# Kernel optimization log

Measured on AMD Instinct MI355X. Metric: run time of the kernel, lower is better.

The kernel has to match this reference:

```python
import jax, jax.numpy as jnp
import numpy as np

B, L, H, DK, DV, DM = 8, 1024, 8, 80, 80, 640
LN_EPS = 1e-5


def setup_inputs() -> dict:
    key = jax.random.key(0)
    ks = jax.random.split(key, 5)
    q = jax.random.normal(ks[0], (B, L, DM), dtype=jnp.float32)
    k = jax.random.normal(ks[1], (B, L, DM), dtype=jnp.float32)
    v = jax.random.normal(ks[2], (B, L, DM), dtype=jnp.float32)
    # fc: nn.Linear(n_head*d_v, d_model), xavier-normal init
    fc_std = float(np.sqrt(2.0 / (H * DV + DM)))
    fc_w = jax.random.normal(ks[3], (DM, H * DV), dtype=jnp.float32) * fc_std
    fc_b = jnp.zeros((DM,), dtype=jnp.float32)
    gamma_1 = jnp.full((DM,), 1e-4, dtype=jnp.float32)  # init_values * ones(640)
    ln_w = jnp.ones((DM,), dtype=jnp.float32)
    ln_b = jnp.zeros((DM,), dtype=jnp.float32)
    return {"q": q, "k": k, "v": v, "fc_w": fc_w, "fc_b": fc_b,
            "gamma_1": gamma_1, "ln_w": ln_w, "ln_b": ln_b}


def reference(q, k, v, fc_w, fc_b, gamma_1, ln_w, ln_b):
    # Inputs are viewed directly into heads (projections are commented out in source).
    residual = q
    qh = q.reshape(B, L, H, DK)  # [b, q, h, d]
    kh = k.reshape(B, L, H, DK)  # [b, k, h, d]
    vh = v.reshape(B, L, H, DV)  # [b, k, h, d]

    # L2-distance attention scores: -sum((q-k)^2) = -(||q||^2 - 2 q.k + ||k||^2)
    sq = jnp.sum(qh * qh, axis=-1)                       # [b, q, h]
    sk = jnp.sum(kh * kh, axis=-1)                       # [b, k, h]
    cross = jnp.einsum('bqhd,bkhd->bhqk', qh, kh)        # [b, h, q, k]
    scores = -(sq.transpose(0, 2, 1)[:, :, :, None]
               - 2.0 * cross
               + sk.transpose(0, 2, 1)[:, :, None, :]) / 13.0

    attn = jax.nn.softmax(scores, axis=-1)               # softmax over keys (dim=2 in 3D view)
    # dropout(p=0.8) treated as identity (eval mode)

    out = jnp.einsum('bhqk,bkhd->bqhd', attn, vh)        # [b, q, h, dv]
    out = out.reshape(B, L, H * DV)
    out = out @ fc_w.T + fc_b                            # fc projection
    # dropout treated as identity (eval mode)

    x = out * gamma_1 + residual
    mu = jnp.mean(x, axis=-1, keepdims=True)
    var = jnp.mean((x - mu) ** 2, axis=-1, keepdims=True)
    y = (x - mu) * jax.lax.rsqrt(var + LN_EPS) * ln_w + ln_b
    return y
```

## Files before the change

kernel.cpp:

```cpp
#include <hip/hip_runtime.h>

#define B_ 8
#define L_ 1024
#define H_ 8
#define DM_ 640

typedef __attribute__((ext_vector_type(8))) short bf16x8;
typedef __attribute__((ext_vector_type(4))) short bf16x4;
typedef __attribute__((ext_vector_type(4))) float f32x4;
typedef __attribute__((ext_vector_type(2))) float f32x2;
typedef __attribute__((ext_vector_type(4))) int i32x4;
typedef __attribute__((ext_vector_type(2))) int i32x2;
typedef __attribute__((ext_vector_type(4))) unsigned short us4;
typedef __attribute__((ext_vector_type(8))) unsigned short us8;

#if __has_builtin(__builtin_amdgcn_exp2f)
#define EXP2F __builtin_amdgcn_exp2f
#else
#define EXP2F exp2f
#endif

#define C1F 0.22195308f
#define C2F 0.11097654f

#define VTP_TILE_SHORTS 5184
#define ATTN8_OFF 10616832

__device__ __forceinline__ unsigned short f2bf(float f) {
  unsigned int u = __builtin_bit_cast(unsigned int, f);
  u += 0x7fffu + ((u >> 16) & 1u);
  return (unsigned short)(u >> 16);
}
__device__ __forceinline__ float bf2f(unsigned short h) {
  unsigned int u = ((unsigned int)h) << 16;
  return __builtin_bit_cast(float, u);
}
__device__ __forceinline__ float sane(float x, float lim) {
  return fminf(fmaxf(x, -lim), lim);
}

__global__ __launch_bounds__(256) void prep_kernel(
    const float* __restrict__ kg, const float* __restrict__ vg,
    unsigned short* __restrict__ Kp, unsigned short* __restrict__ Vtp) {
  __shared__ float V_lds[64 * 81];
  __shared__ float w_lds[64];
  const int tid = threadIdx.x;
  const int bh = blockIdx.x >> 4, kt = blockIdx.x & 15;
  const int b = bh >> 3, h = bh & 7;
  const int key = tid >> 2, part = tid & 3;
  const int keyg = kt * 64 + key;

  const float* krow = kg + (size_t)(b * L_ + keyg) * DM_ + h * 80 + part * 20;
  const float* vrow = vg + (size_t)(b * L_ + keyg) * DM_ + h * 80 + part * 20;
  unsigned short* kpr = Kp + ((size_t)bh * L_ + keyg) * 80 + part * 20;

  float ssq = 0.f;
#pragma unroll
  for (int i = 0; i < 5; ++i) {
    float4 f = *(const float4*)(krow + 4 * i);
    ssq += f.x * f.x + f.y * f.y + f.z * f.z + f.w * f.w;
    us4 h4 = {f2bf(f.x * C1F), f2bf(f.y * C1F), f2bf(f.z * C1F), f2bf(f.w * C1F)};
    *(us4*)(kpr + 4 * i) = h4;
    float4 g4 = *(const float4*)(vrow + 4 * i);
    int d0 = part * 20 + 4 * i;
    V_lds[key * 81 + d0 + 0] = g4.x;
    V_lds[key * 81 + d0 + 1] = g4.y;
    V_lds[key * 81 + d0 + 2] = g4.z;
    V_lds[key * 81 + d0 + 3] = g4.w;
  }
  ssq += __shfl_xor(ssq, 1);
  ssq += __shfl_xor(ssq, 2);
  if (part == 0) w_lds[key] = EXP2F((80.f - ssq) * C2F);
  __syncthreads();

  unsigned short* vt = Vtp + (size_t)(bh * 16 + kt) * VTP_TILE_SHORTS;
#pragma unroll
  for (int r = 0; r < 11; ++r) {
    int p = r * 256 + tid;
    if (p < 81 * 32) {
      int dv = p >> 5, kp = (p & 31) * 2;
      float wa = w_lds[kp], wb = w_lds[kp + 1];
      float va = (dv < 80) ? V_lds[kp * 81 + dv] * wa : wa;
      float vb = (dv < 80) ? V_lds[(kp + 1) * 81 + dv] * wb : wb;
      *(unsigned*)(vt + dv * 64 + kp) =
          (unsigned)f2bf(va) | ((unsigned)f2bf(vb) << 16);
    }
  }
}

#define KSTR 104
#define VSTR 72

__global__ __launch_bounds__(512) void attn_kernel(
    const float* __restrict__ qg, const unsigned short* __restrict__ Kp,
    const unsigned short* __restrict__ Vtp, unsigned char* __restrict__ attn8) {
  __shared__ __align__(16) unsigned short K_lds[2][64 * KSTR];
  __shared__ __align__(16) unsigned short Vt_lds[2][96 * VSTR];

  const int tid = threadIdx.x;
  const int wid = tid >> 6, lane = tid & 63;
  const int col = lane & 15, g = lane >> 4;
  const int g1 = g & 1, g2 = g >> 1;
  const int bx = blockIdx.x;
  const int bh = bx & 63, qt = bx >> 6;
  const int b = bh >> 3, h = bh & 7;

  {
    us8 z = {0, 0, 0, 0, 0, 0, 0, 0};
    if (tid < 128) {
      int bufz = tid >> 6, r = tid & 63;
      *(us8*)&K_lds[bufz][r * KSTR + 80] = z;
      *(us8*)&K_lds[bufz][r * KSTR + 88] = z;
    }
    if (tid < 240) {
      int bufz = tid / 120, t2 = tid % 120;
      int vr = 81 + (t2 >> 3), hc = t2 & 7;
      *(us8*)&Vt_lds[bufz][vr * VSTR + hc * 8] = z;
    }
  }

  const int kr0 = tid / 10, kc0 = tid - kr0 * 10;
  const int idx1 = tid + 512;
  const int kr1 = idx1 / 10, kc1 = idx1 - kr1 * 10;
  const int vr0 = tid >> 3, vc0 = tid & 7;
  const int vr1 = idx1 >> 3, vc1 = idx1 & 7;

  const unsigned short* kslice = Kp + (size_t)bh * L_ * 80;
  const unsigned short* vslice = Vtp + (size_t)(bh * 16) * VTP_TILE_SHORTS;

  us8 sk0, sk1, sv0, sv1;
  auto load_tile = [&](int kt) {
    const unsigned short* kb = kslice + (size_t)kt * 5120;
    const unsigned short* vb = vslice + (size_t)kt * VTP_TILE_SHORTS;
    sk0 = *(const us8*)(kb + kr0 * 80 + kc0 * 8);
    if (tid < 128) sk1 = *(const us8*)(kb + kr1 * 80 + kc1 * 8);
    sv0 = *(const us8*)(vb + vr0 * 64 + vc0 * 8);
    if (tid < 136) sv1 = *(const us8*)(vb + vr1 * 64 + vc1 * 8);
  };
  auto write_tile = [&](int bf) {
    *(us8*)&K_lds[bf][kr0 * KSTR + kc0 * 8] = sk0;
    if (tid < 128) *(us8*)&K_lds[bf][kr1 * KSTR + kc1 * 8] = sk1;
    *(us8*)&Vt_lds[bf][vr0 * VSTR + vc0 * 8] = sv0;
    if (tid < 136) *(us8*)&Vt_lds[bf][vr1 * VSTR + vc1 * 8] = sv1;
  };

  bf16x8 qa[3];
  {
    const int qrow = qt * 128 + wid * 16 + col;
    const float* qr = qg + (size_t)(b * L_ + qrow) * DM_ + h * 80;
#pragma unroll
    for (int c = 0; c < 3; ++c) {
      int d0 = c * 32 + g * 8;
      if (d0 < 80) {
        float4 f0 = *(const float4*)(qr + d0);
        float4 f1 = *(const float4*)(qr + d0 + 4);
        qa[c][0] = (short)f2bf(f0.x); qa[c][1] = (short)f2bf(f0.y);
        qa[c][2] = (short)f2bf(f0.z); qa[c][3] = (short)f2bf(f0.w);
        qa[c][4] = (short)f2bf(f1.x); qa[c][5] = (short)f2bf(f1.y);
        qa[c][6] = (short)f2bf(f1.z); qa[c][7] = (short)f2bf(f1.w);
      } else {
#pragma unroll
        for (int e = 0; e < 8; ++e) qa[c][e] = 0;
      }
    }
  }

  f32x4 acc_o[6];
#pragma unroll
  for (int u = 0; u < 6; ++u) {
    f32x4 z = {0.f, 0.f, 0.f, 0.f};
    acc_o[u] = z;
  }

  load_tile(0);
  write_tile(0);
  __syncthreads();

  for (int kt = 0; kt < 16; ++kt) {
    const int cur = kt & 1;
    if (kt < 15) load_tile(kt + 1);

    f32x4 accS[4];
#pragma unroll
    for (int t = 0; t < 4; ++t) {
      f32x4 z = {0.f, 0.f, 0.f, 0.f};
      accS[t] = z;
    }
#pragma unroll
    for (int t = 0; t < 4; ++t)
#pragma unroll
      for (int c = 0; c < 3; ++c) {
        bf16x8 kf =
            *(const bf16x8*)&K_lds[cur][(t * 16 + col) * KSTR + c * 32 + g * 8];
        accS[t] = __builtin_amdgcn_mfma_f32_16x16x32_bf16(kf, qa[c], accS[t], 0, 0, 0);
      }

    unsigned pkA[4], pkB[4];
#pragma unroll
    for (int t = 0; t < 4; ++t) {
      float p0 = EXP2F(accS[t][0]);
      float p1 = EXP2F(accS[t][1]);
      float p2 = EXP2F(accS[t][2]);
      float p3 = EXP2F(accS[t][3]);
      pkA[t] = (unsigned)f2bf(p0) | ((unsigned)f2bf(p1) << 16);
      pkB[t] = (unsigned)f2bf(p2) | ((unsigned)f2bf(p3) << 16);
    }

#if __has_builtin(__builtin_amdgcn_mfma_f32_16x16x16bf16_1k)
#pragma unroll
    for (int t = 0; t < 4; ++t) {
      i32x2 pw = {(int)pkA[t], (int)pkB[t]};
      bf16x4 pf = __builtin_bit_cast(bf16x4, pw);
#pragma unroll
      for (int u = 0; u < 6; ++u) {
        bf16x4 vf =
            *(const bf16x4*)&Vt_lds[cur][(u * 16 + col) * VSTR + t * 16 + g * 4];
        acc_o[u] =
            __builtin_amdgcn_mfma_f32_16x16x16bf16_1k(vf, pf, acc_o[u], 0, 0, 0);
      }
    }
#else
#pragma unroll
    for (int c = 0; c < 2; ++c) {
      int A0 = pkA[2 * c], A1 = pkA[2 * c + 1];
      int B0 = pkB[2 * c], B1 = pkB[2 * c + 1];
      int a16 = __shfl_xor(A0, 16), a32 = __shfl_xor(A0, 32), a48 = __shfl_xor(A0, 48);
      int c16 = __shfl_xor(A1, 16), c32 = __shfl_xor(A1, 32), c48 = __shfl_xor(A1, 48);
      int b16 = __shfl_xor(B0, 16), b32 = __shfl_xor(B0, 32), b48 = __shfl_xor(B0, 48);
      int d16 = __shfl_xor(B1, 16), d32 = __shfl_xor(B1, 32), d48 = __shfl_xor(B1, 48);
      int W0 = g2 ? (g1 ? c16 : c32) : (g1 ? a48 : A0);
      int W1 = g2 ? (g1 ? d16 : d32) : (g1 ? b48 : B0);
      int W2 = g2 ? (g1 ? A1 : c48) : (g1 ? a32 : a16);
      int W3 = g2 ? (g1 ? B1 : d48) : (g1 ? b32 : b16);
      i32x4 wv = {W0, W1, W2, W3};
      bf16x8 pf = __builtin_bit_cast(bf16x8, wv);
#pragma unroll
      for (int u = 0; u < 6; ++u) {
        bf16x8 vf =
            *(const bf16x8*)&Vt_lds[cur][(u * 16 + col) * VSTR + c * 32 + g * 8];
        acc_o[u] = __builtin_amdgcn_mfma_f32_16x16x32_bf16(vf, pf, acc_o[u], 0, 0, 0);
      }
    }
#endif

    if (kt < 15) {
      write_tile(cur ^ 1);
      __syncthreads();
    }
  }

  float l = __shfl(acc_o[5][0], col);
  float invl = 1.0f / fmaxf(l, 1e-30f);
  const int qrow = qt * 128 + wid * 16 + col;
  unsigned char* ob = attn8 + (size_t)(b * L_ + qrow) * DM_ + h * 80;
#pragma unroll
  for (int u = 0; u < 5; ++u) {
    float o0 = sane(acc_o[u][0] * invl, 240.f);
    float o1 = sane(acc_o[u][1] * invl, 240.f);
    float o2 = sane(acc_o[u][2] * invl, 240.f);
    float o3 = sane(acc_o[u][3] * invl, 240.f);
    int pk = __builtin_amdgcn_cvt_pk_fp8_f32(o0, o1, 0, false);
    pk = __builtin_amdgcn_cvt_pk_fp8_f32(o2, o3, pk, true);
    *(int*)(ob + u * 16 + g * 4) = pk;
  }
}

#define BSTR 40
__global__ __launch_bounds__(256) void fc_kernel(
    const unsigned char* __restrict__ attn8, const float* __restrict__ w,
    const float* __restrict__ fcb, const float* __restrict__ gamma,
    const float* __restrict__ qres, unsigned short* __restrict__ xout) {
  __shared__ __align__(16) unsigned short A_lds[128 * BSTR];
  __shared__ __align__(16) unsigned short B_lds[128 * BSTR];

  const int tid = threadIdx.x;
  const int wid = tid >> 6, lane = tid & 63;
  const int col = lane & 15, g = lane >> 4;
  const int rt = blockIdx.x / 5, ct = blockIdx.x % 5;
  const int wm = wid >> 1, wn = wid & 1;

  f32x4 acc[4][4];
#pragma unroll
  for (int m = 0; m < 4; ++m)
#pragma unroll
    for (int n = 0; n < 4; ++n) {
      f32x4 z = {0.f, 0.f, 0.f, 0.f};
      acc[m][n] = z;
    }

  for (int kc = 0; kc < 20; ++kc) {
    __syncthreads();
    {
      const int r = tid >> 1, seg = tid & 1;
      const unsigned char* as =
          attn8 + (size_t)(rt * 128 + r) * DM_ + kc * 32 + seg * 16;
      uint4 a4 = *(const uint4*)as;
      const unsigned* adw = (const unsigned*)&a4;
#pragma unroll
      for (int wde = 0; wde < 4; ++wde) {
        f32x2 lo = __builtin_amdgcn_cvt_pk_f32_fp8(adw[wde], false);
        f32x2 hi = __builtin_amdgcn_cvt_pk_f32_fp8(adw[wde], true);
        us4 h4 = {f2bf(lo[0]), f2bf(lo[1]), f2bf(hi[0]), f2bf(hi[1])};
        *(us4*)&A_lds[r * BSTR + seg * 16 + wde * 4] = h4;
      }
      const float* wsrc = w + (size_t)(ct * 128 + r) * DM_ + kc * 32 + seg * 16;
#pragma unroll
      for (int i = 0; i < 4; ++i) {
        float4 f = *(const float4*)(wsrc + 4 * i);
        us4 h4 = {f2bf(f.x), f2bf(f.y), f2bf(f.z), f2bf(f.w)};
        *(us4*)&B_lds[r * BSTR + seg * 16 + 4 * i] = h4;
      }
    }
    __syncthreads();

    bf16x8 af[4], bfr[4];
#pragma unroll
    for (int m = 0; m < 4; ++m)
      af[m] = *(const bf16x8*)&A_lds[(wm * 64 + m * 16 + col) * BSTR + g * 8];
#pragma unroll
    for (int n = 0; n < 4; ++n)
      bfr[n] = *(const bf16x8*)&B_lds[(wn * 64 + n * 16 + col) * BSTR + g * 8];
#pragma unroll
    for (int m = 0; m < 4; ++m)
#pragma unroll
      for (int n = 0; n < 4; ++n)
        acc[m][n] = __builtin_amdgcn_mfma_f32_16x16x32_bf16(af[m], bfr[n], acc[m][n], 0, 0, 0);
  }

  int jcol[4];
  float fb4[4], gm[4];
#pragma unroll
  for (int n = 0; n < 4; ++n) {
    jcol[n] = ct * 128 + wn * 64 + n * 16 + col;
    fb4[n] = fcb[jcol[n]];
    gm[n] = gamma[jcol[n]];
  }
#pragma unroll
  for (int m = 0; m < 4; ++m) {
    int rowg = rt * 128 + wm * 64 + m * 16 + g * 4;
#pragma unroll
    for (int j = 0; j < 4; ++j) {
      int row = rowg + j;
#pragma unroll
      for (int n = 0; n < 4; ++n) {
        float xv = (acc[m][n][j] + fb4[n]) * gm[n] + qres[(size_t)row * DM_ + jcol[n]];
        xout[(size_t)row * DM_ + jcol[n]] = f2bf(sane(xv, 1e5f));
      }
    }
  }
}

__global__ __launch_bounds__(256) void ln_kernel(
    const unsigned short* __restrict__ x, const float* __restrict__ lw,
    const float* __restrict__ lb, float* __restrict__ y) {
  const int wid = threadIdx.x >> 6, lane = threadIdx.x & 63;
  const int row = blockIdx.x * 4 + wid;
  const unsigned short* xr = x + (size_t)row * DM_;

  unsigned int u[5];
  float s = 0.f, ss = 0.f;
#pragma unroll
  for (int i = 0; i < 5; ++i) {
    u[i] = *(const unsigned int*)(xr + 2 * (lane + 64 * i));
    float a0 = bf2f((unsigned short)(u[i] & 0xffff));
    float a1 = bf2f((unsigned short)(u[i] >> 16));
    s += a0 + a1;
    ss += a0 * a0 + a1 * a1;
  }
#pragma unroll
  for (int d = 1; d < 64; d <<= 1) {
    s += __shfl_xor(s, d);
    ss += __shfl_xor(ss, d);
  }
  const float mu = s * (1.f / 640.f);
  const float var = ss * (1.f / 640.f) - mu * mu;
  const float rstd = rsqrtf(var + 1e-5f);

  float* yr = y + (size_t)row * DM_;
#pragma unroll
  for (int i = 0; i < 5; ++i) {
    int c0 = 2 * (lane + 64 * i);
    float a0 = bf2f((unsigned short)(u[i] & 0xffff));
    float a1 = bf2f((unsigned short)(u[i] >> 16));
    float2 wv = *(const float2*)(lw + c0);
    float2 bv = *(const float2*)(lb + c0);
    float2 out;
    out.x = (a0 - mu) * rstd * wv.x + bv.x;
    out.y = (a1 - mu) * rstd * wv.y + bv.y;
    *(float2*)(yr + c0) = out;
  }
}

extern "C" void kernel_launch(void* const* d_in, const int* in_sizes, int n_in,
                              void* d_out, int out_size, void* d_ws, size_t ws_size,
                              hipStream_t stream) {
  const float* q = (const float*)d_in[0];
  const float* k = (const float*)d_in[1];
  const float* v = (const float*)d_in[2];
  const float* fw = (const float*)d_in[3];
  const float* fb = (const float*)d_in[4];
  const float* g1 = (const float*)d_in[5];
  const float* lw = (const float*)d_in[6];
  const float* lb = (const float*)d_in[7];

  unsigned short* vtp = (unsigned short*)d_out;
  unsigned char* attn8 = (unsigned char*)d_out + ATTN8_OFF;
  unsigned short* kp = (unsigned short*)d_ws;
  unsigned short* xws = (unsigned short*)d_ws;
  float* y = (float*)d_out;

  prep_kernel<<<dim3(64 * 16), dim3(256), 0, stream>>>(k, v, kp, vtp);
  attn_kernel<<<dim3(64 * 8), dim3(512), 0, stream>>>(q, kp, vtp, attn8);
  fc_kernel<<<dim3((8192 / 128) * 5), dim3(256), 0, stream>>>(attn8, fw, fb, g1, q, xws);
  ln_kernel<<<dim3(8192 / 4), dim3(256), 0, stream>>>(xws, lw, lb, y);
}
```

Measured before the change: 100.9 us.

## Process two query tiles per attention block and double-buffer fc LDS tiles

The attention kernel now handles 256 query rows per block, two 128-row sets sharing each K/V tile loaded into LDS. This halves K/V global and LDS traffic per query, and the grid is halved to 256 blocks. The fc kernel gains double-buffered LDS with register prefetch of the next k-chunk, and the V LDS stride changes from 72 to 76 with a launch-bounds occupancy hint. The trade-off is more registers per thread and fewer blocks (256 on a many-CU GPU), which may underfill the device.

```diff
diff --git a/kernel.cpp b/kernel.cpp
--- a/kernel.cpp
+++ b/kernel.cpp
@@ -89,9 +89,9 @@
 }
 
 #define KSTR 104
-#define VSTR 72
-
-__global__ __launch_bounds__(512) void attn_kernel(
+#define VSTR 76
+
+__global__ __launch_bounds__(512, 2) void attn_kernel(
     const float* __restrict__ qg, const unsigned short* __restrict__ Kp,
     const unsigned short* __restrict__ Vtp, unsigned char* __restrict__ attn8) {
   __shared__ __align__(16) unsigned short K_lds[2][64 * KSTR];
@@ -100,7 +100,6 @@
   const int tid = threadIdx.x;
   const int wid = tid >> 6, lane = tid & 63;
   const int col = lane & 15, g = lane >> 4;
-  const int g1 = g & 1, g2 = g >> 1;
   const int bx = blockIdx.x;
   const int bh = bx & 63, qt = bx >> 6;
   const int b = bh >> 3, h = bh & 7;
@@ -144,32 +143,37 @@
     if (tid < 136) *(us8*)&Vt_lds[bf][vr1 * VSTR + vc1 * 8] = sv1;
   };
 
-  bf16x8 qa[3];
+  bf16x8 qa0[3], qa1[3];
   {
-    const int qrow = qt * 128 + wid * 16 + col;
-    const float* qr = qg + (size_t)(b * L_ + qrow) * DM_ + h * 80;
-#pragma unroll
-    for (int c = 0; c < 3; ++c) {
-      int d0 = c * 32 + g * 8;
-      if (d0 < 80) {
-        float4 f0 = *(const float4*)(qr + d0);
-        float4 f1 = *(const float4*)(qr + d0 + 4);
-        qa[c][0] = (short)f2bf(f0.x); qa[c][1] = (short)f2bf(f0.y);
-        qa[c][2] = (short)f2bf(f0.z); qa[c][3] = (short)f2bf(f0.w);
-        qa[c][4] = (short)f2bf(f1.x); qa[c][5] = (short)f2bf(f1.y);
-        qa[c][6] = (short)f2bf(f1.z); qa[c][7] = (short)f2bf(f1.w);
-      } else {
-#pragma unroll
-        for (int e = 0; e < 8; ++e) qa[c][e] = 0;
+    const int qr0 = qt * 256 + wid * 16 + col;
+#pragma unroll
+    for (int s = 0; s < 2; ++s) {
+      const float* qr = qg + (size_t)(b * L_ + qr0 + s * 128) * DM_ + h * 80;
+      bf16x8* qa = s ? qa1 : qa0;
+#pragma unroll
+      for (int c = 0; c < 3; ++c) {
+        int d0 = c * 32 + g * 8;
+        if (d0 < 80) {
+          float4 f0 = *(const float4*)(qr + d0);
+          float4 f1 = *(const float4*)(qr + d0 + 4);
+          qa[c][0] = (short)f2bf(f0.x); qa[c][1] = (short)f2bf(f0.y);
+          qa[c][2] = (short)f2bf(f0.z); qa[c][3] = (short)f2bf(f0.w);
+          qa[c][4] = (short)f2bf(f1.x); qa[c][5] = (short)f2bf(f1.y);
+          qa[c][6] = (short)f2bf(f1.z); qa[c][7] = (short)f2bf(f1.w);
+        } else {
+#pragma unroll
+          for (int e = 0; e < 8; ++e) qa[c][e] = 0;
+        }
       }
     }
   }
 
-  f32x4 acc_o[6];
+  f32x4 acc_o0[6], acc_o1[6];
 #pragma unroll
   for (int u = 0; u < 6; ++u) {
     f32x4 z = {0.f, 0.f, 0.f, 0.f};
-    acc_o[u] = z;
+    acc_o0[u] = z;
+    acc_o1[u] = z;
   }
 
   load_tile(0);
@@ -180,11 +184,12 @@
     const int cur = kt & 1;
     if (kt < 15) load_tile(kt + 1);
 
-    f32x4 accS[4];
+    f32x4 accS0[4], accS1[4];
 #pragma unroll
     for (int t = 0; t < 4; ++t) {
       f32x4 z = {0.f, 0.f, 0.f, 0.f};
-      accS[t] = z;
+      accS0[t] = z;
+      accS1[t] = z;
     }
 #pragma unroll
     for (int t = 0; t < 4; ++t)
@@ -192,53 +197,65 @@
       for (int c = 0; c < 3; ++c) {
         bf16x8 kf =
             *(const bf16x8*)&K_lds[cur][(t * 16 + col) * KSTR + c * 32 + g * 8];
-        accS[t] = __builtin_amdgcn_mfma_f32_16x16x32_bf16(kf, qa[c], accS[t], 0, 0, 0);
+        accS0[t] = __builtin_amdgcn_mfma_f32_16x16x32_bf16(kf, qa0[c], accS0[t], 0, 0, 0);
+        accS1[t] = __builtin_amdgcn_mfma_f32_16x16x32_bf16(kf, qa1[c], accS1[t], 0, 0, 0);
       }
 
-    unsigned pkA[4], pkB[4];
+    unsigned pkA0[4], pkB0[4], pkA1[4], pkB1[4];
 #pragma unroll
     for (int t = 0; t < 4; ++t) {
-      float p0 = EXP2F(accS[t][0]);
-      float p1 = EXP2F(accS[t][1]);
-      float p2 = EXP2F(accS[t][2]);
-      float p3 = EXP2F(accS[t][3]);
-      pkA[t] = (unsigned)f2bf(p0) | ((unsigned)f2bf(p1) << 16);
-      pkB[t] = (unsigned)f2bf(p2) | ((unsigned)f2bf(p3) << 16);
+      pkA0[t] = (unsigned)f2bf(EXP2F(accS0[t][0])) |
+                ((unsigned)f2bf(EXP2F(accS0[t][1])) << 16);
+      pkB0[t] = (unsigned)f2bf(EXP2F(accS0[t][2])) |
+                ((unsigned)f2bf(EXP2F(accS0[t][3])) << 16);
+      pkA1[t] = (unsigned)f2bf(EXP2F(accS1[t][0])) |
+                ((unsigned)f2bf(EXP2F(accS1[t][1])) << 16);
+      pkB1[t] = (unsigned)f2bf(EXP2F(accS1[t][2])) |
+                ((unsigned)f2bf(EXP2F(accS1[t][3])) << 16);
     }
 
 #if __has_builtin(__builtin_amdgcn_mfma_f32_16x16x16bf16_1k)
 #pragma unroll
     for (int t = 0; t < 4; ++t) {
-      i32x2 pw = {(int)pkA[t], (int)pkB[t]};
-      bf16x4 pf = __builtin_bit_cast(bf16x4, pw);
+      i32x2 pw0 = {(int)pkA0[t], (int)pkB0[t]};
+      i32x2 pw1 = {(int)pkA1[t], (int)pkB1[t]};
+      bf16x4 pf0 = __builtin_bit_cast(bf16x4, pw0);
+      bf16x4 pf1 = __builtin_bit_cast(bf16x4, pw1);
 #pragma unroll
       for (int u = 0; u < 6; ++u) {
         bf16x4 vf =
             *(const bf16x4*)&Vt_lds[cur][(u * 16 + col) * VSTR + t * 16 + g * 4];
-        acc_o[u] =
-            __builtin_amdgcn_mfma_f32_16x16x16bf16_1k(vf, pf, acc_o[u], 0, 0, 0);
+        acc_o0[u] = __builtin_amdgcn_mfma_f32_16x16x16bf16_1k(vf, pf0, acc_o0[u], 0, 0, 0);
+        acc_o1[u] = __builtin_amdgcn_mfma_f32_16x16x16bf16_1k(vf, pf1, acc_o1[u], 0, 0, 0);
       }
     }
 #else
-#pragma unroll
-    for (int c = 0; c < 2; ++c) {
-      int A0 = pkA[2 * c], A1 = pkA[2 * c + 1];
-      int B0 = pkB[2 * c], B1 = pkB[2 * c + 1];
-      int a16 = __shfl_xor(A0, 16), a32 = __shfl_xor(A0, 32), a48 = __shfl_xor(A0, 48);
-      int c16 = __shfl_xor(A1, 16), c32 = __shfl_xor(A1, 32), c48 = __shfl_xor(A1, 48);
-      int b16 = __shfl_xor(B0, 16), b32 = __shfl_xor(B0, 32), b48 = __shfl_xor(B0, 48);
-      int d16 = __shfl_xor(B1, 16), d32 = __shfl_xor(B1, 32), d48 = __shfl_xor(B1, 48);
-      int W0 = g2 ? (g1 ? c16 : c32) : (g1 ? a48 : A0);
-      int W1 = g2 ? (g1 ? d16 : d32) : (g1 ? b48 : B0);
-      int W2 = g2 ? (g1 ? A1 : c48) : (g1 ? a32 : a16);
-      int W3 = g2 ? (g1 ? B1 : d48) : (g1 ? b32 : b16);
-      i32x4 wv = {W0, W1, W2, W3};
-      bf16x8 pf = __builtin_bit_cast(bf16x8, wv);
-#pragma unroll
-      for (int u = 0; u < 6; ++u) {
-        bf16x8 vf =
-            *(const bf16x8*)&Vt_lds[cur][(u * 16 + col) * VSTR + c * 32 + g * 8];
-        acc_o[u] = __builtin_amdgcn_mfma_f32_16x16x32_bf16(vf, pf, acc_o[u], 0, 0, 0);
+    const int g1 = g & 1, g2 = g >> 1;
+#pragma unroll
+    for (int s = 0; s < 2; ++s) {
+      unsigned* pkA = s ? pkA1 : pkA0;
+      unsigned* pkB = s ? pkB1 : pkB0;
+      f32x4* acc_o = s ? acc_o1 : acc_o0;
+#pragma unroll
+      for (int c = 0; c < 2; ++c) {
+        int A0 = pkA[2 * c], A1 = pkA[2 * c + 1];
+        int B0 = pkB[2 * c], B1 = pkB[2 * c + 1];
+        int a16 = __shfl_xor(A0, 16), a32 = __shfl_xor(A0, 32), a48 = __shfl_xor(A0, 48);
+        int c16 = __shfl_xor(A1, 16), c32 = __shfl_xor(A1, 32), c48 = __shfl_xor(A1, 48);
+        int b16 = __shfl_xor(B0, 16), b32 = __shfl_xor(B0, 32), b48 = __shfl_xor(B0, 48);
+        int d16 = __shfl_xor(B1, 16), d32 = __shfl_xor(B1, 32), d48 = __shfl_xor(B1, 48);
+        int W0 = g2 ? (g1 ? c16 : c32) : (g1 ? a48 : A0);
+        int W1 = g2 ? (g1 ? d16 : d32) : (g1 ? b48 : B0);
+        int W2 = g2 ? (g1 ? A1 : c48) : (g1 ? a32 : a16);
+        int W3 = g2 ? (g1 ? B1 : d48) : (g1 ? b32 : b16);
+        i32x4 wv = {W0, W1, W2, W3};
+        bf16x8 pf = __builtin_bit_cast(bf16x8, wv);
+#pragma unroll
+        for (int u = 0; u < 6; ++u) {
+          bf16x8 vf =
+              *(const bf16x8*)&Vt_lds[cur][(u * 16 + col) * VSTR + c * 32 + g * 8];
+          acc_o[u] = __builtin_amdgcn_mfma_f32_16x16x32_bf16(vf, pf, acc_o[u], 0, 0, 0);
+        }
       }
     }
 #endif
@@ -249,19 +266,23 @@
     }
   }
 
-  float l = __shfl(acc_o[5][0], col);
-  float invl = 1.0f / fmaxf(l, 1e-30f);
-  const int qrow = qt * 128 + wid * 16 + col;
-  unsigned char* ob = attn8 + (size_t)(b * L_ + qrow) * DM_ + h * 80;
-#pragma unroll
-  for (int u = 0; u < 5; ++u) {
-    float o0 = sane(acc_o[u][0] * invl, 240.f);
-    float o1 = sane(acc_o[u][1] * invl, 240.f);
-    float o2 = sane(acc_o[u][2] * invl, 240.f);
-    float o3 = sane(acc_o[u][3] * invl, 240.f);
-    int pk = __builtin_amdgcn_cvt_pk_fp8_f32(o0, o1, 0, false);
-    pk = __builtin_amdgcn_cvt_pk_fp8_f32(o2, o3, pk, true);
-    *(int*)(ob + u * 16 + g * 4) = pk;
+#pragma unroll
+  for (int s = 0; s < 2; ++s) {
+    f32x4* acc_o = s ? acc_o1 : acc_o0;
+    float l = __shfl(acc_o[5][0], col);
+    float invl = 1.0f / fmaxf(l, 1e-30f);
+    const int qrow = qt * 256 + s * 128 + wid * 16 + col;
+    unsigned char* ob = attn8 + (size_t)(b * L_ + qrow) * DM_ + h * 80;
+#pragma unroll
+    for (int u = 0; u < 5; ++u) {
+      float o0 = sane(acc_o[u][0] * invl, 240.f);
+      float o1 = sane(acc_o[u][1] * invl, 240.f);
+      float o2 = sane(acc_o[u][2] * invl, 240.f);
+      float o3 = sane(acc_o[u][3] * invl, 240.f);
+      int pk = __builtin_amdgcn_cvt_pk_fp8_f32(o0, o1, 0, false);
+      pk = __builtin_amdgcn_cvt_pk_fp8_f32(o2, o3, pk, true);
+      *(int*)(ob + u * 16 + g * 4) = pk;
+    }
   }
 }
 
@@ -270,14 +291,15 @@
     const unsigned char* __restrict__ attn8, const float* __restrict__ w,
     const float* __restrict__ fcb, const float* __restrict__ gamma,
     const float* __restrict__ qres, unsigned short* __restrict__ xout) {
-  __shared__ __align__(16) unsigned short A_lds[128 * BSTR];
-  __shared__ __align__(16) unsigned short B_lds[128 * BSTR];
+  __shared__ __align__(16) unsigned short A_lds[2][128 * BSTR];
+  __shared__ __align__(16) unsigned short B_lds[2][128 * BSTR];
 
   const int tid = threadIdx.x;
   const int wid = tid >> 6, lane = tid & 63;
   const int col = lane & 15, g = lane >> 4;
   const int rt = blockIdx.x / 5, ct = blockIdx.x % 5;
   const int wm = wid >> 1, wn = wid & 1;
+  const int r = tid >> 1, seg = tid & 1;
 
   f32x4 acc[4][4];
 #pragma unroll
@@ -288,43 +310,55 @@
       acc[m][n] = z;
     }
 
+  uint4 sa;
+  float4 sb[4];
+  auto load_k = [&](int kc) {
+    sa = *(const uint4*)(attn8 + (size_t)(rt * 128 + r) * DM_ + kc * 32 + seg * 16);
+    const float* wsrc = w + (size_t)(ct * 128 + r) * DM_ + kc * 32 + seg * 16;
+#pragma unroll
+    for (int i = 0; i < 4; ++i) sb[i] = *(const float4*)(wsrc + 4 * i);
+  };
+  auto write_k = [&](int bf) {
+    const unsigned* adw = (const unsigned*)&sa;
+#pragma unroll
+    for (int wde = 0; wde < 4; ++wde) {
+      f32x2 lo = __builtin_amdgcn_cvt_pk_f32_fp8(adw[wde], false);
+      f32x2 hi = __builtin_amdgcn_cvt_pk_f32_fp8(adw[wde], true);
+      us4 h4 = {f2bf(lo[0]), f2bf(lo[1]), f2bf(hi[0]), f2bf(hi[1])};
+      *(us4*)&A_lds[bf][r * BSTR + seg * 16 + wde * 4] = h4;
+    }
+#pragma unroll
+    for (int i = 0; i < 4; ++i) {
+      us4 h4 = {f2bf(sb[i].x), f2bf(sb[i].y), f2bf(sb[i].z), f2bf(sb[i].w)};
+      *(us4*)&B_lds[bf][r * BSTR + seg * 16 + 4 * i] = h4;
+    }
+  };
+
+  load_k(0);
+  write_k(0);
+  __syncthreads();
+
   for (int kc = 0; kc < 20; ++kc) {
-    __syncthreads();
-    {
-      const int r = tid >> 1, seg = tid & 1;
-      const unsigned char* as =
-          attn8 + (size_t)(rt * 128 + r) * DM_ + kc * 32 + seg * 16;
-      uint4 a4 = *(const uint4*)as;
-      const unsigned* adw = (const unsigned*)&a4;
-#pragma unroll
-      for (int wde = 0; wde < 4; ++wde) {
-        f32x2 lo = __builtin_amdgcn_cvt_pk_f32_fp8(adw[wde], false);
-        f32x2 hi = __builtin_amdgcn_cvt_pk_f32_fp8(adw[wde], true);
-        us4 h4 = {f2bf(lo[0]), f2bf(lo[1]), f2bf(hi[0]), f2bf(hi[1])};
-        *(us4*)&A_lds[r * BSTR + seg * 16 + wde * 4] = h4;
-      }
-      const float* wsrc = w + (size_t)(ct * 128 + r) * DM_ + kc * 32 + seg * 16;
-#pragma unroll
-      for (int i = 0; i < 4; ++i) {
-        float4 f = *(const float4*)(wsrc + 4 * i);
-        us4 h4 = {f2bf(f.x), f2bf(f.y), f2bf(f.z), f2bf(f.w)};
-        *(us4*)&B_lds[r * BSTR + seg * 16 + 4 * i] = h4;
-      }
-    }
-    __syncthreads();
+    const int cur = kc & 1;
+    if (kc < 19) load_k(kc + 1);
 
     bf16x8 af[4], bfr[4];
 #pragma unroll
     for (int m = 0; m < 4; ++m)
-      af[m] = *(const bf16x8*)&A_lds[(wm * 64 + m * 16 + col) * BSTR + g * 8];
+      af[m] = *(const bf16x8*)&A_lds[cur][(wm * 64 + m * 16 + col) * BSTR + g * 8];
 #pragma unroll
     for (int n = 0; n < 4; ++n)
-      bfr[n] = *(const bf16x8*)&B_lds[(wn * 64 + n * 16 + col) * BSTR + g * 8];
+      bfr[n] = *(const bf16x8*)&B_lds[cur][(wn * 64 + n * 16 + col) * BSTR + g * 8];
 #pragma unroll
     for (int m = 0; m < 4; ++m)
 #pragma unroll
       for (int n = 0; n < 4; ++n)
         acc[m][n] = __builtin_amdgcn_mfma_f32_16x16x32_bf16(af[m], bfr[n], acc[m][n], 0, 0, 0);
+
+    if (kc < 19) {
+      write_k(cur ^ 1);
+      __syncthreads();
+    }
   }
 
   int jcol[4];
@@ -410,7 +444,7 @@
   float* y = (float*)d_out;
 
   prep_kernel<<<dim3(64 * 16), dim3(256), 0, stream>>>(k, v, kp, vtp);
-  attn_kernel<<<dim3(64 * 8), dim3(512), 0, stream>>>(q, kp, vtp, attn8);
+  attn_kernel<<<dim3(64 * 4), dim3(512), 0, stream>>>(q, kp, vtp, attn8);
   fc_kernel<<<dim3((8192 / 128) * 5), dim3(256), 0, stream>>>(attn8, fw, fb, g1, q, xws);
   ln_kernel<<<dim3(8192 / 4), dim3(256), 0, stream>>>(xws, lw, lb, y);
 }
```

New measurement: 88.59 us. -12.2%, faster.
